# Performance work log

Measured on AMD Instinct MI355X. Metric: run time of the kernel, lower is better.

## Reference

```python
import jax, jax.numpy as jnp
import numpy as np

N_TOKENS = 32768
NUM_EMB = 8192
EMB_DIM = 512
COMMITMENT_COST = 0.25


def setup_inputs() -> dict:
    key = jax.random.key(0)
    k1, k2 = jax.random.split(key)
    z_e = jax.random.normal(k1, (N_TOKENS, EMB_DIM), dtype=jnp.float32)
    codebook = jax.random.normal(k2, (NUM_EMB, EMB_DIM), dtype=jnp.float32)
    return {"z_e": z_e, "codebook": codebook}


def reference(z_e, codebook):
    # squared euclidean distances: [N, K]
    distances = (
        jnp.sum(z_e ** 2, axis=1, keepdims=True)
        + jnp.sum(codebook ** 2, axis=1)
        - 2.0 * z_e @ codebook.T
    )
    encoding_indices = jnp.argmin(distances, axis=1)  # [N]
    z_q = codebook[encoding_indices]  # [N, D]

    commitment_loss = jnp.mean((z_e - jax.lax.stop_gradient(z_q)) ** 2)
    vq_loss = COMMITMENT_COST * commitment_loss

    # straight-through estimator
    z_q_st = z_e + jax.lax.stop_gradient(z_q - z_e)
    return z_q_st, vq_loss, commitment_loss, encoding_indices
```

## Files before the change

kernel.cpp:

```cpp
#include <hip/hip_runtime.h>

#define N_TOKENS 32768
#define N_CODES  8192
#define DIM      512

#define BMT 128
#define BNT 128
#define SLICES 4
#define SLICE_CODES (N_CODES / SLICES)
#define NTILES (SLICE_CODES / BNT)
#define BK 64

#define OUT_VQ     16777216
#define OUT_COMMIT 16777217
#define OUT_IDX    16777218

#define WS_CBHI 0
#define WS_CBLO 8388608
#define WS_NC   16777216
#define WS_PART 16809984
#define WS_ACC  17858560
#define WS_ZEHI 18874368
#define WS_ZELO 52428800
#define WS_NEED_FAST 85983232

typedef _Float16 f16x8 __attribute__((ext_vector_type(8)));
typedef _Float16 f16x4 __attribute__((ext_vector_type(4)));
typedef float    f32x4 __attribute__((ext_vector_type(4)));

__device__ __forceinline__ int sw_idx(int row, int kgrp) {
    return row * 64 + ((kgrp ^ (row & 7)) << 3);
}

__device__ __forceinline__ void async_copy16(void* lds, const void* g) {
    __builtin_amdgcn_global_load_lds(
        (const __attribute__((address_space(1))) unsigned int*)g,
        (__attribute__((address_space(3))) unsigned int*)lds,
        16, 0, 0);
}

__global__ void vq_prep_cb_kernel(const float* __restrict__ cb,
                                  _Float16* __restrict__ cb_hi,
                                  _Float16* __restrict__ cb_lo,
                                  float* __restrict__ nc,
                                  float* __restrict__ accum) {
    if (blockIdx.x == 0 && threadIdx.x == 0) *accum = 0.0f;
    const int wid  = threadIdx.x >> 6;
    const int lane = threadIdx.x & 63;
    const int row  = blockIdx.x * 4 + wid;
    const float4* src = (const float4*)(cb + (size_t)row * DIM);
    float4 v0 = src[lane * 2];
    float4 v1 = src[lane * 2 + 1];
    float s = v0.x*v0.x + v0.y*v0.y + v0.z*v0.z + v0.w*v0.w
            + v1.x*v1.x + v1.y*v1.y + v1.z*v1.z + v1.w*v1.w;
    f16x8 hi = {(_Float16)v0.x, (_Float16)v0.y, (_Float16)v0.z, (_Float16)v0.w,
                (_Float16)v1.x, (_Float16)v1.y, (_Float16)v1.z, (_Float16)v1.w};
    f16x8 lo = {(_Float16)(v0.x - (float)hi[0]), (_Float16)(v0.y - (float)hi[1]),
                (_Float16)(v0.z - (float)hi[2]), (_Float16)(v0.w - (float)hi[3]),
                (_Float16)(v1.x - (float)hi[4]), (_Float16)(v1.y - (float)hi[5]),
                (_Float16)(v1.z - (float)hi[6]), (_Float16)(v1.w - (float)hi[7])};
    *(f16x8*)&cb_hi[(size_t)row * DIM + lane * 8] = hi;
    *(f16x8*)&cb_lo[(size_t)row * DIM + lane * 8] = lo;
#pragma unroll
    for (int off = 32; off > 0; off >>= 1) s += __shfl_down(s, off);
    if (lane == 0) nc[row] = s;
}

__global__ void vq_prep_ze_kernel(const float* __restrict__ z_e,
                                  _Float16* __restrict__ ze_hi,
                                  _Float16* __restrict__ ze_lo) {
    const int wid  = threadIdx.x >> 6;
    const int lane = threadIdx.x & 63;
    const int row  = blockIdx.x * 4 + wid;
    const float4* src = (const float4*)(z_e + (size_t)row * DIM);
    float4 v0 = src[lane * 2];
    float4 v1 = src[lane * 2 + 1];
    f16x8 hi = {(_Float16)v0.x, (_Float16)v0.y, (_Float16)v0.z, (_Float16)v0.w,
                (_Float16)v1.x, (_Float16)v1.y, (_Float16)v1.z, (_Float16)v1.w};
    f16x8 lo = {(_Float16)(v0.x - (float)hi[0]), (_Float16)(v0.y - (float)hi[1]),
                (_Float16)(v0.z - (float)hi[2]), (_Float16)(v0.w - (float)hi[3]),
                (_Float16)(v1.x - (float)hi[4]), (_Float16)(v1.y - (float)hi[5]),
                (_Float16)(v1.z - (float)hi[6]), (_Float16)(v1.w - (float)hi[7])};
    *(f16x8*)&ze_hi[(size_t)row * DIM + lane * 8] = hi;
    *(f16x8*)&ze_lo[(size_t)row * DIM + lane * 8] = lo;
}

template <bool PRESPLIT>
__global__ __launch_bounds__(256, 2)
void vq_main_kernel(const float* __restrict__ z_e,
                    const _Float16* __restrict__ ze_hi,
                    const _Float16* __restrict__ ze_lo,
                    const _Float16* __restrict__ cb_hi,
                    const _Float16* __restrict__ cb_lo,
                    const float* __restrict__ nc,
                    float2* __restrict__ partials) {
    __shared__ __align__(16) unsigned char smem[65536];
    _Float16* As_hi = (_Float16*)smem;
    _Float16* As_lo = (_Float16*)(smem + 16384);
    _Float16* Bs_hi = (_Float16*)(smem + 32768);
    _Float16* Bs_lo = (_Float16*)(smem + 49152);

    const int tid    = threadIdx.x;
    const int wid    = tid >> 6;
    const int lane   = tid & 63;
    const int wave_m = wid >> 1;
    const int wave_n = wid & 1;
    const int lane15 = lane & 15;
    const int quad   = lane >> 4;

    const int row0 = blockIdx.x * BMT;
    const int ns   = blockIdx.y;
    const int c00  = ns * SLICE_CODES;

    float minv[4][4];
    int   mini[4][4];
#pragma unroll
    for (int mi = 0; mi < 4; ++mi)
#pragma unroll
        for (int r = 0; r < 4; ++r) { minv[mi][r] = __builtin_inff(); mini[mi][r] = 0; }

    const int s_r0 = tid >> 4;
    const int s_cg = tid & 15;
    const int b_r8 = lane >> 3;
    const int b_g  = lane & 7;

#pragma unroll 1
    for (int nt = 0; nt < NTILES; ++nt) {
        const int c0 = c00 + nt * BNT;
        f32x4 acc[4][4];
#pragma unroll
        for (int mi = 0; mi < 4; ++mi)
#pragma unroll
            for (int ni = 0; ni < 4; ++ni) acc[mi][ni] = (f32x4){0.f, 0.f, 0.f, 0.f};

#pragma unroll 1
        for (int kc = 0; kc < DIM / BK; ++kc) {
            __syncthreads();
#pragma unroll
            for (int i = 0; i < 4; ++i) {
                const int L = wid * 4 + i;
                const int brow = L * 8 + b_r8;
                const size_t goff = (size_t)(c0 + brow) * DIM + kc * BK + ((b_g ^ (brow & 7)) << 3);
                async_copy16(Bs_hi + L * 512, cb_hi + goff);
                async_copy16(Bs_lo + L * 512, cb_lo + goff);
            }
            if constexpr (PRESPLIT) {
#pragma unroll
                for (int i = 0; i < 4; ++i) {
                    const int L = wid * 4 + i;
                    const int arow = L * 8 + b_r8;
                    const size_t goff = (size_t)(row0 + arow) * DIM + kc * BK + ((b_g ^ (arow & 7)) << 3);
                    async_copy16(As_hi + L * 512, ze_hi + goff);
                    async_copy16(As_lo + L * 512, ze_lo + goff);
                }
            } else {
#pragma unroll
                for (int rr = 0; rr < 8; ++rr) {
                    const int row = rr * 16 + s_r0;
                    float4 v = *(const float4*)&z_e[(size_t)(row0 + row) * DIM + kc * BK + s_cg * 4];
                    f16x4 hi = {(_Float16)v.x, (_Float16)v.y, (_Float16)v.z, (_Float16)v.w};
                    f16x4 lo = {(_Float16)(v.x - (float)hi[0]), (_Float16)(v.y - (float)hi[1]),
                                (_Float16)(v.z - (float)hi[2]), (_Float16)(v.w - (float)hi[3])};
                    const int a = sw_idx(row, s_cg >> 1) + ((s_cg & 1) << 2);
                    *(f16x4*)&As_hi[a] = hi;
                    *(f16x4*)&As_lo[a] = lo;
                }
            }
            __syncthreads();

#pragma unroll
            for (int ks = 0; ks < 2; ++ks) {
                const int kg = ks * 4 + quad;
                f16x8 ah[4], al[4], bh[4], bl[4];
#pragma unroll
                for (int mi = 0; mi < 4; ++mi) {
                    const int a = sw_idx(wave_m * 64 + mi * 16 + lane15, kg);
                    ah[mi] = *(const f16x8*)&As_hi[a];
                    al[mi] = *(const f16x8*)&As_lo[a];
                }
#pragma unroll
                for (int ni = 0; ni < 4; ++ni) {
                    const int b = sw_idx(wave_n * 64 + ni * 16 + lane15, kg);
                    bh[ni] = *(const f16x8*)&Bs_hi[b];
                    bl[ni] = *(const f16x8*)&Bs_lo[b];
                }
#pragma unroll
                for (int mi = 0; mi < 4; ++mi)
#pragma unroll
                    for (int ni = 0; ni < 4; ++ni)
                        acc[mi][ni] = __builtin_amdgcn_mfma_f32_16x16x32_f16(ah[mi], bh[ni], acc[mi][ni], 0, 0, 0);
#pragma unroll
                for (int mi = 0; mi < 4; ++mi)
#pragma unroll
                    for (int ni = 0; ni < 4; ++ni)
                        acc[mi][ni] = __builtin_amdgcn_mfma_f32_16x16x32_f16(al[mi], bh[ni], acc[mi][ni], 0, 0, 0);
#pragma unroll
                for (int mi = 0; mi < 4; ++mi)
#pragma unroll
                    for (int ni = 0; ni < 4; ++ni)
                        acc[mi][ni] = __builtin_amdgcn_mfma_f32_16x16x32_f16(ah[mi], bl[ni], acc[mi][ni], 0, 0, 0);
            }
        }

#pragma unroll
        for (int ni = 0; ni < 4; ++ni) {
            const int c = c0 + wave_n * 64 + ni * 16 + lane15;
            const float nrm = nc[c];
#pragma unroll
            for (int mi = 0; mi < 4; ++mi)
#pragma unroll
                for (int r = 0; r < 4; ++r) {
                    const float v = fmaf(-2.0f, acc[mi][ni][r], nrm);
                    if (v < minv[mi][r]) { minv[mi][r] = v; mini[mi][r] = c; }
                }
        }
    }

    __syncthreads();
    float* redv = (float*)smem;
    int*   redi = (int*)(smem + 16384);
#pragma unroll
    for (int mi = 0; mi < 4; ++mi)
#pragma unroll
        for (int r = 0; r < 4; ++r) {
            const int rl = wave_m * 64 + mi * 16 + quad * 4 + r;
            const int o = wave_n * 2048 + rl * 16 + lane15;
            redv[o] = minv[mi][r];
            redi[o] = mini[mi][r];
        }
    __syncthreads();
    if (tid < BMT) {
        float bv = __builtin_inff();
        int   bi = 0x7fffffff;
        for (int j = 0; j < 32; ++j) {
            const int o = (j >= 16 ? 2048 : 0) + tid * 16 + (j & 15);
            const float v = redv[o];
            const int   i = redi[o];
            if (v < bv || (v == bv && i < bi)) { bv = v; bi = i; }
        }
        partials[(size_t)(row0 + tid) * SLICES + ns] = make_float2(bv, __int_as_float(bi));
    }
}

__global__ void vq_merge_kernel(const float* __restrict__ z_e,
                                const float* __restrict__ cb,
                                const float2* __restrict__ partials,
                                float* __restrict__ out,
                                float* __restrict__ accum) {
    __shared__ float wpart[4];
    const int wid  = threadIdx.x >> 6;
    const int lane = threadIdx.x & 63;
    const int tbase = blockIdx.x * 64 + wid * 16;
    float part = 0.0f;
#pragma unroll 1
    for (int t = 0; t < 16; ++t) {
        const int token = tbase + t;
        float bv = __builtin_inff();
        int   bi = 0;
#pragma unroll
        for (int s = 0; s < SLICES; ++s) {
            float2 p = partials[(size_t)token * SLICES + s];
            if (p.x < bv) { bv = p.x; bi = __float_as_int(p.y); }
        }
        const int code = bi & (N_CODES - 1);
        const float4* zp = (const float4*)(z_e + (size_t)token * DIM);
        const float4* cp = (const float4*)(cb + (size_t)code * DIM);
        float4* op = (float4*)out + (size_t)token * (DIM / 4);
#pragma unroll
        for (int i = 0; i < 2; ++i) {
            const int e = lane + i * 64;
            float4 z = zp[e];
            float4 q = cp[e];
            op[e] = q;
            float dx = z.x - q.x, dy = z.y - q.y, dz = z.z - q.z, dw = z.w - q.w;
            part += dx * dx + dy * dy + dz * dz + dw * dw;
        }
        if (lane == 0) out[OUT_IDX + token] = (float)code;
    }
#pragma unroll
    for (int off = 32; off > 0; off >>= 1) part += __shfl_down(part, off);
    if (lane == 0) wpart[wid] = part;
    __syncthreads();
    if (threadIdx.x == 0) atomicAdd(accum, wpart[0] + wpart[1] + wpart[2] + wpart[3]);
}

__global__ void vq_finalize_kernel(const float* __restrict__ accum,
                                   float* __restrict__ out) {
    const float c = *accum * (1.0f / (float)(N_TOKENS * DIM));
    out[OUT_VQ]     = 0.25f * c;
    out[OUT_COMMIT] = c;
}

extern "C" void kernel_launch(void* const* d_in, const int* in_sizes, int n_in,
                              void* d_out, int out_size, void* d_ws, size_t ws_size,
                              hipStream_t stream) {
    const float* z_e = (const float*)d_in[0];
    const float* cb  = (const float*)d_in[1];
    float* out = (float*)d_out;

    _Float16* cb_hi = (_Float16*)((char*)d_ws + WS_CBHI);
    _Float16* cb_lo = (_Float16*)((char*)d_ws + WS_CBLO);
    float*    nc    = (float*)((char*)d_ws + WS_NC);
    float2*   part  = (float2*)((char*)d_ws + WS_PART);
    float*    accum = (float*)((char*)d_ws + WS_ACC);
    _Float16* ze_hi = (_Float16*)((char*)d_ws + WS_ZEHI);
    _Float16* ze_lo = (_Float16*)((char*)d_ws + WS_ZELO);

    const bool fast = (ws_size >= (size_t)WS_NEED_FAST);

    hipLaunchKernelGGL(vq_prep_cb_kernel, dim3(N_CODES / 4), dim3(256), 0, stream,
                       cb, cb_hi, cb_lo, nc, accum);
    if (fast) {
        hipLaunchKernelGGL(vq_prep_ze_kernel, dim3(N_TOKENS / 4), dim3(256), 0, stream,
                           z_e, ze_hi, ze_lo);
        hipLaunchKernelGGL((vq_main_kernel<true>), dim3(N_TOKENS / BMT, SLICES), dim3(256), 0, stream,
                           z_e, ze_hi, ze_lo, cb_hi, cb_lo, nc, part);
    } else {
        hipLaunchKernelGGL((vq_main_kernel<false>), dim3(N_TOKENS / BMT, SLICES), dim3(256), 0, stream,
                           z_e, ze_hi, ze_lo, cb_hi, cb_lo, nc, part);
    }
    hipLaunchKernelGGL(vq_merge_kernel, dim3(N_TOKENS / 64), dim3(256), 0, stream,
                       z_e, cb, part, out, accum);
    hipLaunchKernelGGL(vq_finalize_kernel, dim3(1), dim3(1), 0, stream, accum, out);
}
```

Baseline: 867.6 us.

## Double-buffer LDS tiles with BK=32 and remap blocks for XCD locality

Replaces the single-buffered K loop (two barriers per chunk) with a flattened double-buffered pipeline. The next BK=32 chunk is loaded asynchronously into the other half of shared memory while the MFMAs run on the current one, with one barrier per step. It also adds a new swizzle for 32-wide rows and remaps block IDs so each XCD handles one codebook slice, aiming for better L2 reuse. The risk is that halving BK doubles the number of barriers and steps, and the async loads may not be waited on correctly before the next barrier.

```diff
diff --git a/kernel.cpp b/kernel.cpp
--- a/kernel.cpp
+++ b/kernel.cpp
@@ -9,7 +9,9 @@
 #define SLICES 4
 #define SLICE_CODES (N_CODES / SLICES)
 #define NTILES (SLICE_CODES / BNT)
-#define BK 64
+#define BK 32
+#define CHUNKS (DIM / BK)
+#define STEPS (NTILES * CHUNKS)
 
 #define OUT_VQ     16777216
 #define OUT_COMMIT 16777217
@@ -28,8 +30,8 @@
 typedef _Float16 f16x4 __attribute__((ext_vector_type(4)));
 typedef float    f32x4 __attribute__((ext_vector_type(4)));
 
-__device__ __forceinline__ int sw_idx(int row, int kgrp) {
-    return row * 64 + ((kgrp ^ (row & 7)) << 3);
+__device__ __forceinline__ int sw32(int row, int kgrp) {
+    return row * 32 + (((kgrp ^ ((row >> 1) & 3))) << 3);
 }
 
 __device__ __forceinline__ void async_copy16(void* lds, const void* g) {
@@ -95,10 +97,6 @@
                     const float* __restrict__ nc,
                     float2* __restrict__ partials) {
     __shared__ __align__(16) unsigned char smem[65536];
-    _Float16* As_hi = (_Float16*)smem;
-    _Float16* As_lo = (_Float16*)(smem + 16384);
-    _Float16* Bs_hi = (_Float16*)(smem + 32768);
-    _Float16* Bs_lo = (_Float16*)(smem + 49152);
 
     const int tid    = threadIdx.x;
     const int wid    = tid >> 6;
@@ -108,9 +106,62 @@
     const int lane15 = lane & 15;
     const int quad   = lane >> 4;
 
-    const int row0 = blockIdx.x * BMT;
-    const int ns   = blockIdx.y;
+    const int bid  = blockIdx.x + gridDim.x * blockIdx.y;
+    const int xcd  = bid & 7;
+    const int ns   = xcd >> 1;
+    const int mt   = ((xcd & 1) << 7) | (bid >> 3);
+    const int row0 = mt * BMT;
     const int c00  = ns * SLICE_CODES;
+
+    int aoff[4], boff[4];
+#pragma unroll
+    for (int i = 0; i < 4; ++i) {
+        const int ra = wave_m * 64 + i * 16 + lane15;
+        aoff[i] = sw32(ra, quad);
+        const int rb = wave_n * 64 + i * 16 + lane15;
+        boff[i] = sw32(rb, quad);
+    }
+
+    const int r4 = lane >> 2;
+    const int sl = lane & 3;
+    const int s_r0 = tid >> 3;
+    const int s_cg = tid & 7;
+
+    auto stage = [&](int buf, int step) {
+        const int nt = step >> 4;
+        const int kc = step & 15;
+        const int c0 = c00 + nt * BNT;
+        _Float16* base = (_Float16*)(smem + buf * 32768);
+#pragma unroll
+        for (int i = 0; i < 2; ++i) {
+            const int L   = wid * 2 + i;
+            const int row = L * 16 + r4;
+            const int g   = sl ^ ((row >> 1) & 3);
+            const size_t kb = (size_t)(c0 + row) * DIM + kc * BK + g * 8;
+            async_copy16(base + 8192  + L * 512, cb_hi + kb);
+            async_copy16(base + 12288 + L * 512, cb_lo + kb);
+            if constexpr (PRESPLIT) {
+                const size_t ka = (size_t)(row0 + row) * DIM + kc * BK + g * 8;
+                async_copy16(base +        L * 512, ze_hi + ka);
+                async_copy16(base + 4096 + L * 512, ze_lo + ka);
+            }
+        }
+        if constexpr (!PRESPLIT) {
+            _Float16* Ah = base;
+            _Float16* Al = base + 4096;
+#pragma unroll
+            for (int rr = 0; rr < 4; ++rr) {
+                const int row = rr * 32 + s_r0;
+                float4 v = *(const float4*)&z_e[(size_t)(row0 + row) * DIM + kc * BK + s_cg * 4];
+                f16x4 hi = {(_Float16)v.x, (_Float16)v.y, (_Float16)v.z, (_Float16)v.w};
+                f16x4 lo = {(_Float16)(v.x - (float)hi[0]), (_Float16)(v.y - (float)hi[1]),
+                            (_Float16)(v.z - (float)hi[2]), (_Float16)(v.w - (float)hi[3])};
+                const int a = sw32(row, s_cg >> 1) + ((s_cg & 1) << 2);
+                *(f16x4*)&Ah[a] = hi;
+                *(f16x4*)&Al[a] = lo;
+            }
+        }
+    };
 
     float minv[4][4];
     int   mini[4][4];
@@ -119,101 +170,69 @@
 #pragma unroll
         for (int r = 0; r < 4; ++r) { minv[mi][r] = __builtin_inff(); mini[mi][r] = 0; }
 
-    const int s_r0 = tid >> 4;
-    const int s_cg = tid & 15;
-    const int b_r8 = lane >> 3;
-    const int b_g  = lane & 7;
+    f32x4 acc[4][4];
+    int buf = 0;
+    stage(0, 0);
 
 #pragma unroll 1
-    for (int nt = 0; nt < NTILES; ++nt) {
-        const int c0 = c00 + nt * BNT;
-        f32x4 acc[4][4];
+    for (int step = 0; step < STEPS; ++step) {
+        const int nt = step >> 4;
+        const int kc = step & 15;
+        if (kc == 0) {
+#pragma unroll
+            for (int mi = 0; mi < 4; ++mi)
+#pragma unroll
+                for (int ni = 0; ni < 4; ++ni) acc[mi][ni] = (f32x4){0.f, 0.f, 0.f, 0.f};
+        }
+
+        __syncthreads();
+
+        if (step + 1 < STEPS) stage(buf ^ 1, step + 1);
+
+        _Float16* base = (_Float16*)(smem + buf * 32768);
+        f16x8 ah[4], al[4], bh[4], bl[4];
+#pragma unroll
+        for (int mi = 0; mi < 4; ++mi) {
+            ah[mi] = *(const f16x8*)&base[aoff[mi]];
+            al[mi] = *(const f16x8*)&base[4096 + aoff[mi]];
+        }
+#pragma unroll
+        for (int ni = 0; ni < 4; ++ni) {
+            bh[ni] = *(const f16x8*)&base[8192 + boff[ni]];
+            bl[ni] = *(const f16x8*)&base[12288 + boff[ni]];
+        }
 #pragma unroll
         for (int mi = 0; mi < 4; ++mi)
 #pragma unroll
-            for (int ni = 0; ni < 4; ++ni) acc[mi][ni] = (f32x4){0.f, 0.f, 0.f, 0.f};
-
-#pragma unroll 1
-        for (int kc = 0; kc < DIM / BK; ++kc) {
-            __syncthreads();
-#pragma unroll
-            for (int i = 0; i < 4; ++i) {
-                const int L = wid * 4 + i;
-                const int brow = L * 8 + b_r8;
-                const size_t goff = (size_t)(c0 + brow) * DIM + kc * BK + ((b_g ^ (brow & 7)) << 3);
-                async_copy16(Bs_hi + L * 512, cb_hi + goff);
-                async_copy16(Bs_lo + L * 512, cb_lo + goff);
+            for (int ni = 0; ni < 4; ++ni)
+                acc[mi][ni] = __builtin_amdgcn_mfma_f32_16x16x32_f16(ah[mi], bh[ni], acc[mi][ni], 0, 0, 0);
+#pragma unroll
+        for (int mi = 0; mi < 4; ++mi)
+#pragma unroll
+            for (int ni = 0; ni < 4; ++ni)
+                acc[mi][ni] = __builtin_amdgcn_mfma_f32_16x16x32_f16(al[mi], bh[ni], acc[mi][ni], 0, 0, 0);
+#pragma unroll
+        for (int mi = 0; mi < 4; ++mi)
+#pragma unroll
+            for (int ni = 0; ni < 4; ++ni)
+                acc[mi][ni] = __builtin_amdgcn_mfma_f32_16x16x32_f16(ah[mi], bl[ni], acc[mi][ni], 0, 0, 0);
+
+        if (kc == 15) {
+            const int c0 = c00 + nt * BNT;
+#pragma unroll
+            for (int ni = 0; ni < 4; ++ni) {
+                const int c = c0 + wave_n * 64 + ni * 16 + lane15;
+                const float nrm = nc[c];
+#pragma unroll
+                for (int mi = 0; mi < 4; ++mi)
+#pragma unroll
+                    for (int r = 0; r < 4; ++r) {
+                        const float v = fmaf(-2.0f, acc[mi][ni][r], nrm);
+                        if (v < minv[mi][r]) { minv[mi][r] = v; mini[mi][r] = c; }
+                    }
             }
-            if constexpr (PRESPLIT) {
-#pragma unroll
-                for (int i = 0; i < 4; ++i) {
-                    const int L = wid * 4 + i;
-                    const int arow = L * 8 + b_r8;
-                    const size_t goff = (size_t)(row0 + arow) * DIM + kc * BK + ((b_g ^ (arow & 7)) << 3);
-                    async_copy16(As_hi + L * 512, ze_hi + goff);
-                    async_copy16(As_lo + L * 512, ze_lo + goff);
-                }
-            } else {
-#pragma unroll
-                for (int rr = 0; rr < 8; ++rr) {
-                    const int row = rr * 16 + s_r0;
-                    float4 v = *(const float4*)&z_e[(size_t)(row0 + row) * DIM + kc * BK + s_cg * 4];
-                    f16x4 hi = {(_Float16)v.x, (_Float16)v.y, (_Float16)v.z, (_Float16)v.w};
-                    f16x4 lo = {(_Float16)(v.x - (float)hi[0]), (_Float16)(v.y - (float)hi[1]),
-                                (_Float16)(v.z - (float)hi[2]), (_Float16)(v.w - (float)hi[3])};
-                    const int a = sw_idx(row, s_cg >> 1) + ((s_cg & 1) << 2);
-                    *(f16x4*)&As_hi[a] = hi;
-                    *(f16x4*)&As_lo[a] = lo;
-                }
-            }
-            __syncthreads();
-
-#pragma unroll
-            for (int ks = 0; ks < 2; ++ks) {
-                const int kg = ks * 4 + quad;
-                f16x8 ah[4], al[4], bh[4], bl[4];
-#pragma unroll
-                for (int mi = 0; mi < 4; ++mi) {
-                    const int a = sw_idx(wave_m * 64 + mi * 16 + lane15, kg);
-                    ah[mi] = *(const f16x8*)&As_hi[a];
-                    al[mi] = *(const f16x8*)&As_lo[a];
-                }
-#pragma unroll
-                for (int ni = 0; ni < 4; ++ni) {
-                    const int b = sw_idx(wave_n * 64 + ni * 16 + lane15, kg);
-                    bh[ni] = *(const f16x8*)&Bs_hi[b];
-                    bl[ni] = *(const f16x8*)&Bs_lo[b];
-                }
-#pragma unroll
-                for (int mi = 0; mi < 4; ++mi)
-#pragma unroll
-                    for (int ni = 0; ni < 4; ++ni)
-                        acc[mi][ni] = __builtin_amdgcn_mfma_f32_16x16x32_f16(ah[mi], bh[ni], acc[mi][ni], 0, 0, 0);
-#pragma unroll
-                for (int mi = 0; mi < 4; ++mi)
-#pragma unroll
-                    for (int ni = 0; ni < 4; ++ni)
-                        acc[mi][ni] = __builtin_amdgcn_mfma_f32_16x16x32_f16(al[mi], bh[ni], acc[mi][ni], 0, 0, 0);
-#pragma unroll
-                for (int mi = 0; mi < 4; ++mi)
-#pragma unroll
-                    for (int ni = 0; ni < 4; ++ni)
-                        acc[mi][ni] = __builtin_amdgcn_mfma_f32_16x16x32_f16(ah[mi], bl[ni], acc[mi][ni], 0, 0, 0);
-            }
-        }
-
-#pragma unroll
-        for (int ni = 0; ni < 4; ++ni) {
-            const int c = c0 + wave_n * 64 + ni * 16 + lane15;
-            const float nrm = nc[c];
-#pragma unroll
-            for (int mi = 0; mi < 4; ++mi)
-#pragma unroll
-                for (int r = 0; r < 4; ++r) {
-                    const float v = fmaf(-2.0f, acc[mi][ni][r], nrm);
-                    if (v < minv[mi][r]) { minv[mi][r] = v; mini[mi][r] = c; }
-                }
-        }
+        }
+        buf ^= 1;
     }
 
     __syncthreads();
```

Measured after the change: 909.9 us. 4.9% more time.

## Screen with fp16-hi GEMM plus error bound, recompute uncertain tokens exactly

Applied to the files above, without the earlier changes.

Replaces the full three-term split-fp16 distance GEMM with a single hi-only fp16 GEMM that tracks the best and second-best distance per slice. A certification pass uses norm-based error bounds from the hi/lo split to accept tokens whose winner is provably separated, refining the few surviving candidates in fp32. Tokens that fail certification are appended to a list and rerun through the exact hi/lo kernel plus a final merge. This is meant to cut the MFMA and load work of the main GEMM, at the cost of extra kernels, atomics and an exact fallback whose size depends on the data.

```diff
diff --git a/kernel.cpp b/kernel.cpp
--- a/kernel.cpp
+++ b/kernel.cpp
@@ -10,18 +10,26 @@
 #define SLICE_CODES (N_CODES / SLICES)
 #define NTILES (SLICE_CODES / BNT)
 #define BK 64
+#define CHUNKS (DIM / BK)
+
+#define CAP_FLAG 32768
+#define SLACK 0.25f
 
 #define OUT_VQ     16777216
 #define OUT_COMMIT 16777217
 #define OUT_IDX    16777218
 
-#define WS_CBHI 0
-#define WS_CBLO 8388608
-#define WS_NC   16777216
-#define WS_PART 16809984
-#define WS_ACC  17858560
-#define WS_ZEHI 18874368
-#define WS_ZELO 52428800
+#define WS_CBHI   0
+#define WS_CBLO   8388608
+#define WS_NC     16777216
+#define WS_NORMZ  16809984
+#define WS_MISC   17072128
+#define WS_LIST   17072144
+#define WS_PARTV1 17301504
+#define WS_PARTI1 17825792
+#define WS_PARTV2 18350080
+#define WS_ZEHI   18874368
+#define WS_ZELO   52428800
 #define WS_NEED_FAST 85983232
 
 typedef _Float16 f16x8 __attribute__((ext_vector_type(8)));
@@ -39,12 +47,15 @@
         16, 0, 0);
 }
 
+__global__ void vq_init_kernel(unsigned int* misc) {
+    if (threadIdx.x < 4) misc[threadIdx.x] = 0u;
+}
+
 __global__ void vq_prep_cb_kernel(const float* __restrict__ cb,
                                   _Float16* __restrict__ cb_hi,
                                   _Float16* __restrict__ cb_lo,
                                   float* __restrict__ nc,
-                                  float* __restrict__ accum) {
-    if (blockIdx.x == 0 && threadIdx.x == 0) *accum = 0.0f;
+                                  unsigned int* __restrict__ misc) {
     const int wid  = threadIdx.x >> 6;
     const int lane = threadIdx.x & 63;
     const int row  = blockIdx.x * 4 + wid;
@@ -55,20 +66,33 @@
             + v1.x*v1.x + v1.y*v1.y + v1.z*v1.z + v1.w*v1.w;
     f16x8 hi = {(_Float16)v0.x, (_Float16)v0.y, (_Float16)v0.z, (_Float16)v0.w,
                 (_Float16)v1.x, (_Float16)v1.y, (_Float16)v1.z, (_Float16)v1.w};
-    f16x8 lo = {(_Float16)(v0.x - (float)hi[0]), (_Float16)(v0.y - (float)hi[1]),
-                (_Float16)(v0.z - (float)hi[2]), (_Float16)(v0.w - (float)hi[3]),
-                (_Float16)(v1.x - (float)hi[4]), (_Float16)(v1.y - (float)hi[5]),
-                (_Float16)(v1.z - (float)hi[6]), (_Float16)(v1.w - (float)hi[7])};
+    float h0=(float)hi[0], h1=(float)hi[1], h2=(float)hi[2], h3=(float)hi[3];
+    float h4=(float)hi[4], h5=(float)hi[5], h6=(float)hi[6], h7=(float)hi[7];
+    float l0=v0.x-h0, l1=v0.y-h1, l2=v0.z-h2, l3=v0.w-h3;
+    float l4=v1.x-h4, l5=v1.y-h5, l6=v1.z-h6, l7=v1.w-h7;
+    f16x8 lo = {(_Float16)l0,(_Float16)l1,(_Float16)l2,(_Float16)l3,
+                (_Float16)l4,(_Float16)l5,(_Float16)l6,(_Float16)l7};
     *(f16x8*)&cb_hi[(size_t)row * DIM + lane * 8] = hi;
     *(f16x8*)&cb_lo[(size_t)row * DIM + lane * 8] = lo;
-#pragma unroll
-    for (int off = 32; off > 0; off >>= 1) s += __shfl_down(s, off);
-    if (lane == 0) nc[row] = s;
+    float sh = h0*h0+h1*h1+h2*h2+h3*h3+h4*h4+h5*h5+h6*h6+h7*h7;
+    float sl = l0*l0+l1*l1+l2*l2+l3*l3+l4*l4+l5*l5+l6*l6+l7*l7;
+#pragma unroll
+    for (int off = 32; off > 0; off >>= 1) {
+        s  += __shfl_down(s, off);
+        sh += __shfl_down(sh, off);
+        sl += __shfl_down(sl, off);
+    }
+    if (lane == 0) {
+        nc[row] = s;
+        atomicMax(&misc[0], __float_as_uint(sl));
+        atomicMax(&misc[1], __float_as_uint(sh));
+    }
 }
 
 __global__ void vq_prep_ze_kernel(const float* __restrict__ z_e,
                                   _Float16* __restrict__ ze_hi,
-                                  _Float16* __restrict__ ze_lo) {
+                                  _Float16* __restrict__ ze_lo,
+                                  float2* __restrict__ normz) {
     const int wid  = threadIdx.x >> 6;
     const int lane = threadIdx.x & 63;
     const int row  = blockIdx.x * 4 + wid;
@@ -77,28 +101,33 @@
     float4 v1 = src[lane * 2 + 1];
     f16x8 hi = {(_Float16)v0.x, (_Float16)v0.y, (_Float16)v0.z, (_Float16)v0.w,
                 (_Float16)v1.x, (_Float16)v1.y, (_Float16)v1.z, (_Float16)v1.w};
-    f16x8 lo = {(_Float16)(v0.x - (float)hi[0]), (_Float16)(v0.y - (float)hi[1]),
-                (_Float16)(v0.z - (float)hi[2]), (_Float16)(v0.w - (float)hi[3]),
-                (_Float16)(v1.x - (float)hi[4]), (_Float16)(v1.y - (float)hi[5]),
-                (_Float16)(v1.z - (float)hi[6]), (_Float16)(v1.w - (float)hi[7])};
+    float h0=(float)hi[0], h1=(float)hi[1], h2=(float)hi[2], h3=(float)hi[3];
+    float h4=(float)hi[4], h5=(float)hi[5], h6=(float)hi[6], h7=(float)hi[7];
+    float l0=v0.x-h0, l1=v0.y-h1, l2=v0.z-h2, l3=v0.w-h3;
+    float l4=v1.x-h4, l5=v1.y-h5, l6=v1.z-h6, l7=v1.w-h7;
+    f16x8 lo = {(_Float16)l0,(_Float16)l1,(_Float16)l2,(_Float16)l3,
+                (_Float16)l4,(_Float16)l5,(_Float16)l6,(_Float16)l7};
     *(f16x8*)&ze_hi[(size_t)row * DIM + lane * 8] = hi;
     *(f16x8*)&ze_lo[(size_t)row * DIM + lane * 8] = lo;
-}
-
-template <bool PRESPLIT>
+    float sh = h0*h0+h1*h1+h2*h2+h3*h3+h4*h4+h5*h5+h6*h6+h7*h7;
+    float sl = l0*l0+l1*l1+l2*l2+l3*l3+l4*l4+l5*l5+l6*l6+l7*l7;
+#pragma unroll
+    for (int off = 32; off > 0; off >>= 1) {
+        sh += __shfl_down(sh, off);
+        sl += __shfl_down(sl, off);
+    }
+    if (lane == 0) normz[row] = make_float2(sh, sl);
+}
+
 __global__ __launch_bounds__(256, 2)
-void vq_main_kernel(const float* __restrict__ z_e,
-                    const _Float16* __restrict__ ze_hi,
-                    const _Float16* __restrict__ ze_lo,
-                    const _Float16* __restrict__ cb_hi,
-                    const _Float16* __restrict__ cb_lo,
-                    const float* __restrict__ nc,
-                    float2* __restrict__ partials) {
-    __shared__ __align__(16) unsigned char smem[65536];
-    _Float16* As_hi = (_Float16*)smem;
-    _Float16* As_lo = (_Float16*)(smem + 16384);
-    _Float16* Bs_hi = (_Float16*)(smem + 32768);
-    _Float16* Bs_lo = (_Float16*)(smem + 49152);
+void vq_main_hi_kernel(const _Float16* __restrict__ ze_hi,
+                       const _Float16* __restrict__ cb_hi,
+                       const float* __restrict__ nc,
+                       float* __restrict__ pv1, int* __restrict__ pi1,
+                       float* __restrict__ pv2) {
+    __shared__ __align__(16) unsigned char smem[49152];
+    _Float16* As = (_Float16*)smem;
+    _Float16* Bs = (_Float16*)smem + 8192;
 
     const int tid    = threadIdx.x;
     const int wid    = tid >> 6;
@@ -108,19 +137,20 @@
     const int lane15 = lane & 15;
     const int quad   = lane >> 4;
 
+    const int ns   = blockIdx.y;
     const int row0 = blockIdx.x * BMT;
-    const int ns   = blockIdx.y;
     const int c00  = ns * SLICE_CODES;
 
-    float minv[4][4];
-    int   mini[4][4];
+    float minv1[4][4], minv2[4][4];
+    int   mini1[4][4];
 #pragma unroll
     for (int mi = 0; mi < 4; ++mi)
 #pragma unroll
-        for (int r = 0; r < 4; ++r) { minv[mi][r] = __builtin_inff(); mini[mi][r] = 0; }
-
-    const int s_r0 = tid >> 4;
-    const int s_cg = tid & 15;
+        for (int r = 0; r < 4; ++r) {
+            minv1[mi][r] = __builtin_inff(); minv2[mi][r] = __builtin_inff();
+            mini1[mi][r] = 0;
+        }
+
     const int b_r8 = lane >> 3;
     const int b_g  = lane & 7;
 
@@ -134,24 +164,244 @@
             for (int ni = 0; ni < 4; ++ni) acc[mi][ni] = (f32x4){0.f, 0.f, 0.f, 0.f};
 
 #pragma unroll 1
-        for (int kc = 0; kc < DIM / BK; ++kc) {
+        for (int kc = 0; kc < CHUNKS; ++kc) {
+            __syncthreads();
+#pragma unroll
+            for (int i = 0; i < 4; ++i) {
+                const int L = wid * 4 + i;
+                const int row = L * 8 + b_r8;
+                const int g = (b_g ^ (row & 7)) << 3;
+                async_copy16(Bs + L * 512, cb_hi + (size_t)(c0 + row) * DIM + kc * BK + g);
+                async_copy16(As + L * 512, ze_hi + (size_t)(row0 + row) * DIM + kc * BK + g);
+            }
+            __syncthreads();
+
+#pragma unroll
+            for (int ks = 0; ks < 2; ++ks) {
+                const int kg = ks * 4 + quad;
+                f16x8 ah[4], bh[4];
+#pragma unroll
+                for (int mi = 0; mi < 4; ++mi)
+                    ah[mi] = *(const f16x8*)&As[sw_idx(wave_m * 64 + mi * 16 + lane15, kg)];
+#pragma unroll
+                for (int ni = 0; ni < 4; ++ni)
+                    bh[ni] = *(const f16x8*)&Bs[sw_idx(wave_n * 64 + ni * 16 + lane15, kg)];
+#pragma unroll
+                for (int mi = 0; mi < 4; ++mi)
+#pragma unroll
+                    for (int ni = 0; ni < 4; ++ni)
+                        acc[mi][ni] = __builtin_amdgcn_mfma_f32_16x16x32_f16(
+                            ah[mi], bh[ni], acc[mi][ni], 0, 0, 0);
+            }
+        }
+
+#pragma unroll
+        for (int ni = 0; ni < 4; ++ni) {
+            const int c = c0 + wave_n * 64 + ni * 16 + lane15;
+            const float nrm = nc[c];
+#pragma unroll
+            for (int mi = 0; mi < 4; ++mi)
+#pragma unroll
+                for (int r = 0; r < 4; ++r) {
+                    const float v = fmaf(-2.0f, acc[mi][ni][r], nrm);
+                    if (v < minv1[mi][r]) {
+                        minv2[mi][r] = minv1[mi][r];
+                        minv1[mi][r] = v; mini1[mi][r] = c;
+                    } else if (v < minv2[mi][r]) {
+                        minv2[mi][r] = v;
+                    }
+                }
+        }
+    }
+
+    __syncthreads();
+    float* rv1 = (float*)smem;
+    int*   ri1 = (int*)(smem + 16384);
+    float* rv2 = (float*)(smem + 32768);
+#pragma unroll
+    for (int mi = 0; mi < 4; ++mi)
+#pragma unroll
+        for (int r = 0; r < 4; ++r) {
+            const int rl = wave_m * 64 + mi * 16 + quad * 4 + r;
+            const int o = wave_n * 2048 + rl * 16 + lane15;
+            rv1[o] = minv1[mi][r]; ri1[o] = mini1[mi][r]; rv2[o] = minv2[mi][r];
+        }
+    __syncthreads();
+    if (tid < BMT) {
+        float bv1 = __builtin_inff(), bv2 = __builtin_inff();
+        int   bi1 = 0x7fffffff;
+        for (int j = 0; j < 32; ++j) {
+            const int o = (j >= 16 ? 2048 : 0) + tid * 16 + (j & 15);
+            const float v1 = rv1[o]; const int i1 = ri1[o]; const float v2 = rv2[o];
+            if (v1 < bv1 || (v1 == bv1 && i1 < bi1)) {
+                bv2 = fminf(fminf(bv1, v2), bv2);
+                bv1 = v1; bi1 = i1;
+            } else {
+                bv2 = fminf(bv2, v1);
+            }
+        }
+        const size_t p = (size_t)(row0 + tid) * SLICES + ns;
+        pv1[p] = bv1; pi1[p] = bi1; pv2[p] = bv2;
+    }
+}
+
+__global__ void vq_merge_cert_kernel(const float* __restrict__ z_e,
+                                     const float* __restrict__ cb,
+                                     const float* __restrict__ nc,
+                                     const float* __restrict__ pv1,
+                                     const int* __restrict__ pi1,
+                                     const float* __restrict__ pv2,
+                                     const float2* __restrict__ normz,
+                                     unsigned int* __restrict__ misc,
+                                     int* __restrict__ list,
+                                     float* __restrict__ out,
+                                     float* __restrict__ accum) {
+    __shared__ float wpart[4];
+    const int wid  = threadIdx.x >> 6;
+    const int lane = threadIdx.x & 63;
+    const int tbase = blockIdx.x * 64 + wid * 16;
+    const float maxCl = sqrtf(__uint_as_float(misc[0]));
+    const float maxCh = sqrtf(__uint_as_float(misc[1]));
+    int* flagcnt = (int*)&misc[2];
+    float part = 0.0f;
+
+#pragma unroll 1
+    for (int t = 0; t < 16; ++t) {
+        const int token = tbase + t;
+        float m1[4], m2[4]; int i1[4];
+#pragma unroll
+        for (int s = 0; s < 4; ++s) {
+            const size_t p = (size_t)token * SLICES + s;
+            m1[s] = pv1[p]; i1[s] = pi1[p]; m2[s] = pv2[p];
+        }
+        float g1 = m1[0]; int gi = i1[0];
+#pragma unroll
+        for (int s = 1; s < 4; ++s)
+            if (m1[s] < g1 || (m1[s] == g1 && i1[s] < gi)) { g1 = m1[s]; gi = i1[s]; }
+
+        const float2 nz = normz[token];
+        const float Bnd = 2.0f * (sqrtf(nz.x) * maxCl + sqrtf(nz.y) * (maxCh + maxCl)) + SLACK;
+        const float thresh = g1 + 2.0f * Bnd;
+        const bool cert = (m2[0] > thresh) && (m2[1] > thresh) &&
+                          (m2[2] > thresh) && (m2[3] > thresh);
+        if (!cert) {
+            if (lane == 0) { const int pos = atomicAdd(flagcnt, 1); list[pos] = token; }
+        } else {
+            const float4* zp = (const float4*)(z_e + (size_t)token * DIM);
+            const float4 z0 = zp[lane], z1 = zp[lane + 64];
+            float best = __builtin_inff(); int bc = 0x7fffffff;
+#pragma unroll 1
+            for (int s = 0; s < 4; ++s) {
+                if (m1[s] <= thresh) {
+                    const int c = i1[s];
+                    const float4* cp = (const float4*)(cb + (size_t)c * DIM);
+                    const float4 c0v = cp[lane], c1v = cp[lane + 64];
+                    float p = z0.x*c0v.x + z0.y*c0v.y + z0.z*c0v.z + z0.w*c0v.w
+                            + z1.x*c1v.x + z1.y*c1v.y + z1.z*c1v.z + z1.w*c1v.w;
+#pragma unroll
+                    for (int off = 32; off > 0; off >>= 1) p += __shfl_down(p, off);
+                    p = __shfl(p, 0);
+                    const float sx = fmaf(-2.0f, p, nc[c]);
+                    if (sx < best || (sx == best && c < bc)) { best = sx; bc = c; }
+                }
+            }
+            const float4* cp = (const float4*)(cb + (size_t)bc * DIM);
+            const float4 q0 = cp[lane], q1 = cp[lane + 64];
+            float4* op = (float4*)out + (size_t)token * (DIM / 4);
+            op[lane] = q0; op[lane + 64] = q1;
+            float dx = z0.x-q0.x, dy = z0.y-q0.y, dz = z0.z-q0.z, dw = z0.w-q0.w;
+            part += dx*dx + dy*dy + dz*dz + dw*dw;
+            dx = z1.x-q1.x; dy = z1.y-q1.y; dz = z1.z-q1.z; dw = z1.w-q1.w;
+            part += dx*dx + dy*dy + dz*dz + dw*dw;
+            if (lane == 0) out[OUT_IDX + token] = (float)bc;
+        }
+    }
+#pragma unroll
+    for (int off = 32; off > 0; off >>= 1) part += __shfl_down(part, off);
+    if (lane == 0) wpart[wid] = part;
+    __syncthreads();
+    if (threadIdx.x == 0) atomicAdd(accum, wpart[0] + wpart[1] + wpart[2] + wpart[3]);
+}
+
+template <bool INDIRECT, bool PRESPLIT>
+__global__ __launch_bounds__(256, 2)
+void vq_exact_kernel(const float* __restrict__ z_e,
+                     const _Float16* __restrict__ ze_hi,
+                     const _Float16* __restrict__ ze_lo,
+                     const _Float16* __restrict__ cb_hi,
+                     const _Float16* __restrict__ cb_lo,
+                     const float* __restrict__ nc,
+                     const int* __restrict__ list,
+                     const int* __restrict__ pcnt,
+                     float2* __restrict__ fpart) {
+    int n;
+    if constexpr (INDIRECT) { n = *pcnt; if (n > CAP_FLAG) n = CAP_FLAG; }
+    else n = N_TOKENS;
+    const int row0 = blockIdx.x * BMT;
+    if (row0 >= n) return;
+
+    __shared__ __align__(16) unsigned char smem[65536];
+    _Float16* As_hi = (_Float16*)smem;
+    _Float16* As_lo = (_Float16*)(smem + 16384);
+    _Float16* Bs_hi = (_Float16*)(smem + 32768);
+    _Float16* Bs_lo = (_Float16*)(smem + 49152);
+
+    const int tid    = threadIdx.x;
+    const int wid    = tid >> 6;
+    const int lane   = tid & 63;
+    const int wave_m = wid >> 1;
+    const int wave_n = wid & 1;
+    const int lane15 = lane & 15;
+    const int quad   = lane >> 4;
+
+    const int ns  = blockIdx.y;
+    const int c00 = ns * SLICE_CODES;
+
+    float minv[4][4];
+    int   mini[4][4];
+#pragma unroll
+    for (int mi = 0; mi < 4; ++mi)
+#pragma unroll
+        for (int r = 0; r < 4; ++r) { minv[mi][r] = __builtin_inff(); mini[mi][r] = 0; }
+
+    const int b_r8 = lane >> 3;
+    const int b_g  = lane & 7;
+    const int s_r0 = tid >> 4;
+    const int s_cg = tid & 15;
+
+#pragma unroll 1
+    for (int nt = 0; nt < NTILES; ++nt) {
+        const int c0 = c00 + nt * BNT;
+        f32x4 acc[4][4];
+#pragma unroll
+        for (int mi = 0; mi < 4; ++mi)
+#pragma unroll
+            for (int ni = 0; ni < 4; ++ni) acc[mi][ni] = (f32x4){0.f, 0.f, 0.f, 0.f};
+
+#pragma unroll 1
+        for (int kc = 0; kc < CHUNKS; ++kc) {
             __syncthreads();
 #pragma unroll
             for (int i = 0; i < 4; ++i) {
                 const int L = wid * 4 + i;
                 const int brow = L * 8 + b_r8;
-                const size_t goff = (size_t)(c0 + brow) * DIM + kc * BK + ((b_g ^ (brow & 7)) << 3);
-                async_copy16(Bs_hi + L * 512, cb_hi + goff);
-                async_copy16(Bs_lo + L * 512, cb_lo + goff);
+                const size_t kb = (size_t)(c0 + brow) * DIM + kc * BK + ((b_g ^ (brow & 7)) << 3);
+                async_copy16(Bs_hi + L * 512, cb_hi + kb);
+                async_copy16(Bs_lo + L * 512, cb_lo + kb);
             }
             if constexpr (PRESPLIT) {
 #pragma unroll
                 for (int i = 0; i < 4; ++i) {
                     const int L = wid * 4 + i;
                     const int arow = L * 8 + b_r8;
-                    const size_t goff = (size_t)(row0 + arow) * DIM + kc * BK + ((b_g ^ (arow & 7)) << 3);
-                    async_copy16(As_hi + L * 512, ze_hi + goff);
-                    async_copy16(As_lo + L * 512, ze_lo + goff);
+                    int tok;
+                    if constexpr (INDIRECT) {
+                        const int pos = row0 + arow;
+                        tok = (pos < n) ? list[pos] : 0;
+                    } else tok = row0 + arow;
+                    const size_t ka = (size_t)tok * DIM + kc * BK + ((b_g ^ (arow & 7)) << 3);
+                    async_copy16(As_hi + L * 512, ze_hi + ka);
+                    async_copy16(As_lo + L * 512, ze_lo + ka);
                 }
             } else {
 #pragma unroll
@@ -238,44 +488,56 @@
             const int   i = redi[o];
             if (v < bv || (v == bv && i < bi)) { bv = v; bi = i; }
         }
-        partials[(size_t)(row0 + tid) * SLICES + ns] = make_float2(bv, __int_as_float(bi));
-    }
-}
-
-__global__ void vq_merge_kernel(const float* __restrict__ z_e,
-                                const float* __restrict__ cb,
-                                const float2* __restrict__ partials,
-                                float* __restrict__ out,
-                                float* __restrict__ accum) {
+        fpart[(size_t)(row0 + tid) * SLICES + ns] = make_float2(bv, __int_as_float(bi));
+    }
+}
+
+template <bool INDIRECT>
+__global__ void vq_final_merge_kernel(const float* __restrict__ z_e,
+                                      const float* __restrict__ cb,
+                                      const float2* __restrict__ fpart,
+                                      const int* __restrict__ list,
+                                      const int* __restrict__ pcnt,
+                                      float* __restrict__ out,
+                                      float* __restrict__ accum) {
     __shared__ float wpart[4];
+    int n;
+    if constexpr (INDIRECT) { n = *pcnt; if (n > CAP_FLAG) n = CAP_FLAG; }
+    else n = N_TOKENS;
     const int wid  = threadIdx.x >> 6;
     const int lane = threadIdx.x & 63;
     const int tbase = blockIdx.x * 64 + wid * 16;
     float part = 0.0f;
 #pragma unroll 1
     for (int t = 0; t < 16; ++t) {
-        const int token = tbase + t;
-        float bv = __builtin_inff();
-        int   bi = 0;
-#pragma unroll
-        for (int s = 0; s < SLICES; ++s) {
-            float2 p = partials[(size_t)token * SLICES + s];
-            if (p.x < bv) { bv = p.x; bi = __float_as_int(p.y); }
-        }
-        const int code = bi & (N_CODES - 1);
-        const float4* zp = (const float4*)(z_e + (size_t)token * DIM);
-        const float4* cp = (const float4*)(cb + (size_t)code * DIM);
-        float4* op = (float4*)out + (size_t)token * (DIM / 4);
-#pragma unroll
-        for (int i = 0; i < 2; ++i) {
-            const int e = lane + i * 64;
-            float4 z = zp[e];
-            float4 q = cp[e];
-            op[e] = q;
-            float dx = z.x - q.x, dy = z.y - q.y, dz = z.z - q.z, dw = z.w - q.w;
-            part += dx * dx + dy * dy + dz * dz + dw * dw;
-        }
-        if (lane == 0) out[OUT_IDX + token] = (float)code;
+        const int pos = tbase + t;
+        const bool valid = pos < n;
+        if (valid) {
+            int token;
+            if constexpr (INDIRECT) token = list[pos]; else token = pos;
+            float bv = __builtin_inff();
+            int   bi = 0x7fffffff;
+#pragma unroll
+            for (int s = 0; s < SLICES; ++s) {
+                float2 p = fpart[(size_t)pos * SLICES + s];
+                const float v = p.x; const int i = __float_as_int(p.y);
+                if (v < bv || (v == bv && i < bi)) { bv = v; bi = i; }
+            }
+            const int code = bi & (N_CODES - 1);
+            const float4* zp = (const float4*)(z_e + (size_t)token * DIM);
+            const float4* cp = (const float4*)(cb + (size_t)code * DIM);
+            float4* op = (float4*)out + (size_t)token * (DIM / 4);
+#pragma unroll
+            for (int i = 0; i < 2; ++i) {
+                const int e = lane + i * 64;
+                float4 z = zp[e];
+                float4 q = cp[e];
+                op[e] = q;
+                float dx = z.x - q.x, dy = z.y - q.y, dz = z.z - q.z, dw = z.w - q.w;
+                part += dx * dx + dy * dy + dz * dz + dw * dw;
+            }
+            if (lane == 0) out[OUT_IDX + token] = (float)code;
+        }
     }
 #pragma unroll
     for (int off = 32; off > 0; off >>= 1) part += __shfl_down(part, off);
@@ -298,28 +560,42 @@
     const float* cb  = (const float*)d_in[1];
     float* out = (float*)d_out;
 
-    _Float16* cb_hi = (_Float16*)((char*)d_ws + WS_CBHI);
-    _Float16* cb_lo = (_Float16*)((char*)d_ws + WS_CBLO);
-    float*    nc    = (float*)((char*)d_ws + WS_NC);
-    float2*   part  = (float2*)((char*)d_ws + WS_PART);
-    float*    accum = (float*)((char*)d_ws + WS_ACC);
-    _Float16* ze_hi = (_Float16*)((char*)d_ws + WS_ZEHI);
-    _Float16* ze_lo = (_Float16*)((char*)d_ws + WS_ZELO);
+    _Float16*     cb_hi  = (_Float16*)((char*)d_ws + WS_CBHI);
+    _Float16*     cb_lo  = (_Float16*)((char*)d_ws + WS_CBLO);
+    float*        nc     = (float*)((char*)d_ws + WS_NC);
+    float2*       normz  = (float2*)((char*)d_ws + WS_NORMZ);
+    unsigned int* misc   = (unsigned int*)((char*)d_ws + WS_MISC);
+    int*          list   = (int*)((char*)d_ws + WS_LIST);
+    float*        pv1    = (float*)((char*)d_ws + WS_PARTV1);
+    int*          pi1    = (int*)((char*)d_ws + WS_PARTI1);
+    float*        pv2    = (float*)((char*)d_ws + WS_PARTV2);
+    float2*       fpart  = (float2*)((char*)d_ws + WS_PARTV1);
+    _Float16*     ze_hi  = (_Float16*)((char*)d_ws + WS_ZEHI);
+    _Float16*     ze_lo  = (_Float16*)((char*)d_ws + WS_ZELO);
+    int*          flagcnt = (int*)&misc[2];
+    float*        accum   = (float*)&misc[3];
 
     const bool fast = (ws_size >= (size_t)WS_NEED_FAST);
 
+    hipLaunchKernelGGL(vq_init_kernel, dim3(1), dim3(64), 0, stream, misc);
     hipLaunchKernelGGL(vq_prep_cb_kernel, dim3(N_CODES / 4), dim3(256), 0, stream,
-                       cb, cb_hi, cb_lo, nc, accum);
+                       cb, cb_hi, cb_lo, nc, misc);
     if (fast) {
         hipLaunchKernelGGL(vq_prep_ze_kernel, dim3(N_TOKENS / 4), dim3(256), 0, stream,
-                           z_e, ze_hi, ze_lo);
-        hipLaunchKernelGGL((vq_main_kernel<true>), dim3(N_TOKENS / BMT, SLICES), dim3(256), 0, stream,
-                           z_e, ze_hi, ze_lo, cb_hi, cb_lo, nc, part);
+                           z_e, ze_hi, ze_lo, normz);
+        hipLaunchKernelGGL(vq_main_hi_kernel, dim3(N_TOKENS / BMT, SLICES), dim3(256), 0, stream,
+                           ze_hi, cb_hi, nc, pv1, pi1, pv2);
+        hipLaunchKernelGGL(vq_merge_cert_kernel, dim3(N_TOKENS / 64), dim3(256), 0, stream,
+                           z_e, cb, nc, pv1, pi1, pv2, normz, misc, list, out, accum);
+        hipLaunchKernelGGL((vq_exact_kernel<true, true>), dim3(CAP_FLAG / BMT, SLICES), dim3(256), 0, stream,
+                           z_e, ze_hi, ze_lo, cb_hi, cb_lo, nc, list, flagcnt, fpart);
+        hipLaunchKernelGGL((vq_final_merge_kernel<true>), dim3(CAP_FLAG / 64), dim3(256), 0, stream,
+                           z_e, cb, fpart, list, flagcnt, out, accum);
     } else {
-        hipLaunchKernelGGL((vq_main_kernel<false>), dim3(N_TOKENS / BMT, SLICES), dim3(256), 0, stream,
-                           z_e, ze_hi, ze_lo, cb_hi, cb_lo, nc, part);
-    }
-    hipLaunchKernelGGL(vq_merge_kernel, dim3(N_TOKENS / 64), dim3(256), 0, stream,
-                       z_e, cb, part, out, accum);
+        hipLaunchKernelGGL((vq_exact_kernel<false, false>), dim3(N_TOKENS / BMT, SLICES), dim3(256), 0, stream,
+                           z_e, ze_hi, ze_lo, cb_hi, cb_lo, nc, (const int*)nullptr, (const int*)nullptr, fpart);
+        hipLaunchKernelGGL((vq_final_merge_kernel<false>), dim3(N_TOKENS / 64), dim3(256), 0, stream,
+                           z_e, cb, fpart, (const int*)nullptr, (const int*)nullptr, out, accum);
+    }
     hipLaunchKernelGGL(vq_finalize_kernel, dim3(1), dim3(1), 0, stream, accum, out);
 }
```

New measurement: 1.079 ms. +24.3%, slower.
